# Kernel tuning notes

Hardware: AMD Instinct MI355X
Metric: run time of the kernel (lower is better)

Reference implementation:

```python
import jax, jax.numpy as jnp
import numpy as np

TEMPERATURE = 8.0  # sqrt(head_dim=64)
NEG_FILL = -1000000000.0

def setup_inputs() -> dict:
    key = jax.random.key(0)
    k1, k2, k3, k4, k5 = jax.random.split(key, 5)
    B, H, S, D = 4, 16, 1024, 64
    q = jax.random.normal(k1, (B, H, S, D), dtype=jnp.float32)
    k = jax.random.normal(k2, (B, H, S, D), dtype=jnp.float32)
    v = jax.random.normal(k3, (B, H, S, D), dtype=jnp.float32)
    similarity = jax.random.normal(k4, (B, H, S, S), dtype=jnp.float32)
    mask = jax.random.randint(k5, (B, 1, S, S), 0, 2).astype(bool)
    return {"q": q, "k": k, "v": v, "similarity": similarity, "mask": mask}

def reference(q, k, v, similarity, mask):
    # scores: [B,H,S,S] = (q/temp) @ k^T
    attn = jnp.einsum('bhqd,bhkd->bhqk', q / TEMPERATURE, k)
    attn = jnp.where(mask, NEG_FILL, attn)          # masked_fill (mask broadcasts over heads)
    attn = jax.nn.softmax(attn + similarity, axis=-1)  # dropout p=0 (eval): identity
    output = jnp.einsum('bhqk,bhkd->bhqd', attn, v)
    return (output, attn)
```

## Files before the change

### kernel.cpp

```cpp
#include <hip/hip_runtime.h>
#include <stdint.h>


#define S_LEN 1024
#define D_DIM 64
#define QT 16
#define SSTR 1032
#define NEG_FILL (-1000000000.0f)
#define LOG2E 1.44269504088896340736f

typedef __bf16 bf16x8 __attribute__((ext_vector_type(8)));
typedef float f32x4 __attribute__((ext_vector_type(4)));
typedef unsigned short u16x4 __attribute__((ext_vector_type(4)));
typedef unsigned short u16x8 __attribute__((ext_vector_type(8)));

__device__ __forceinline__ unsigned short f2bf(float x) {
    unsigned u = __builtin_bit_cast(unsigned, x);
    u += 0x7fffu + ((u >> 16) & 1u);
    return (unsigned short)(u >> 16);
}
__device__ __forceinline__ float bf2f(unsigned short b) {
    return __builtin_bit_cast(float, (unsigned)b << 16);
}

__global__ void prep_qkm(const float* __restrict__ q, const float* __restrict__ k,
                         const void* __restrict__ mraw,
                         unsigned short* __restrict__ Qb, unsigned short* __restrict__ Kb,
                         unsigned char* __restrict__ Mb)
{
    const int t = threadIdx.x;
    const int i = blockIdx.x * 256 + t;
    f32x4 q4 = ((const f32x4*)q)[i];
    f32x4 k4 = ((const f32x4*)k)[i];
    u16x4 qo, ko;
#pragma unroll
    for (int j = 0; j < 4; ++j) {
        qo[j] = f2bf(q4[j] * 0.125f);
        ko[j] = f2bf(k4[j]);
    }
    ((u16x4*)Qb)[i] = qo;
    ((u16x4*)Kb)[i] = ko;

    __shared__ int s_not_int, s_not_f32;
    if (t == 0) { s_not_int = 0; s_not_f32 = 0; }
    __syncthreads();
    const unsigned* wdd = (const unsigned*)mraw;
    int ni = 0, nf = 0;
    for (int j = t; j < 1024; j += 256) {
        unsigned x = wdd[j];
        if (x > 1u) ni = 1;
        if (x != 0u && x != 0x3f800000u) nf = 1;
    }
    if (ni) s_not_int = 1;
    if (nf) s_not_f32 = 1;
    __syncthreads();
    const int fmt = (s_not_int == 0) ? 0 : ((s_not_f32 == 0) ? 1 : 2);
    uchar4 o;
    if (fmt == 0) {
        int4 x = ((const int4*)mraw)[i];
        o.x = x.x ? 1 : 0; o.y = x.y ? 1 : 0; o.z = x.z ? 1 : 0; o.w = x.w ? 1 : 0;
    } else if (fmt == 1) {
        float4 x = ((const float4*)mraw)[i];
        o.x = (x.x != 0.f) ? 1 : 0; o.y = (x.y != 0.f) ? 1 : 0;
        o.z = (x.z != 0.f) ? 1 : 0; o.w = (x.w != 0.f) ? 1 : 0;
    } else {
        uchar4 x = ((const uchar4*)mraw)[i];
        o.x = x.x ? 1 : 0; o.y = x.y ? 1 : 0; o.z = x.z ? 1 : 0; o.w = x.w ? 1 : 0;
    }
    ((uchar4*)Mb)[i] = o;
}

__global__ void prep_vt(const float* __restrict__ v, unsigned short* __restrict__ Vt)
{
    __shared__ unsigned short sT[64 * 72];
    const int bh = blockIdx.x >> 4;
    const int st = blockIdx.x & 15;
    const int t = threadIdx.x;
    const float* vb = v + (size_t)(bh * S_LEN + st * 64) * D_DIM;
#pragma unroll
    for (int p = 0; p < 4; ++p) {
        int lin = p * 256 + t;
        int r = lin >> 4;
        int c = lin & 15;
        f32x4 x = ((const f32x4*)(vb + r * D_DIM))[c];
        unsigned short* dst = &sT[r * 72 + c * 4];
#pragma unroll
        for (int j = 0; j < 4; ++j) dst[j] = f2bf(x[j]);
    }
    __syncthreads();
    unsigned short* ob = Vt + (size_t)bh * D_DIM * S_LEN + st * 64;
#pragma unroll
    for (int p = 0; p < 4; ++p) {
        int lin = p * 256 + t;
        int d = lin >> 4;
        int s4 = (lin & 15) * 4;
        u16x4 o;
#pragma unroll
        for (int j = 0; j < 4; ++j) o[j] = sT[(s4 + j) * 72 + d];
        *(u16x4*)&ob[d * S_LEN + s4] = o;
    }
}

__global__ __launch_bounds__(256, 4)
void attn_main(const float* __restrict__ simg_, const unsigned short* __restrict__ Qb,
               const unsigned short* __restrict__ Kb, const unsigned short* __restrict__ Vtb,
               const unsigned char* __restrict__ Mb, float* __restrict__ out,
               float* __restrict__ attn)
{
    __shared__ __align__(16) unsigned short sS[QT * SSTR];

    const int blk = blockIdx.x;
    const int bh = blk >> 6;
    const int qt = blk & 63;
    const int b = bh >> 4;
    const int t = threadIdx.x;
    const int w = t >> 6;
    const int lane = t & 63;
    const int quad = lane >> 4;
    const int l15 = lane & 15;

    const unsigned short* Qg = Qb + (size_t)(bh * S_LEN + qt * QT) * D_DIM;
    const unsigned short* Kg = Kb + (size_t)bh * S_LEN * D_DIM;
    const unsigned short* Vg = Vtb + (size_t)bh * D_DIM * S_LEN;
    const float* simg = simg_ + ((size_t)(bh * S_LEN + qt * QT)) * S_LEN;
    const unsigned char* mg = Mb + ((size_t)(b * S_LEN + qt * QT)) * S_LEN;
    float* attng = attn + ((size_t)(bh * S_LEN + qt * QT)) * S_LEN;

    const int n0 = w * 16;
    const bf16x8 av0 = *(const bf16x8*)&Qg[l15 * D_DIM + quad * 8];
    const bf16x8 av1 = *(const bf16x8*)&Qg[l15 * D_DIM + 32 + quad * 8];
#pragma unroll 4
    for (int kt = 0; kt < 16; ++kt) {
        const unsigned short* kp = &Kg[(size_t)(kt * 64 + n0 + l15) * D_DIM + quad * 8];
        bf16x8 bv0 = *(const bf16x8*)kp;
        bf16x8 bv1 = *(const bf16x8*)(kp + 32);
        f32x4 acc = {0.f, 0.f, 0.f, 0.f};
        acc = __builtin_amdgcn_mfma_f32_16x16x32_bf16(av0, bv0, acc, 0, 0, 0);
        acc = __builtin_amdgcn_mfma_f32_16x16x32_bf16(av1, bv1, acc, 0, 0, 0);
        const int colg = kt * 64 + n0 + l15;
#pragma unroll
        for (int r = 0; r < 4; ++r)
            sS[(quad * 4 + r) * SSTR + colg] = f2bf(acc[r]);
    }
    __syncthreads();

#pragma unroll 1
    for (int rr = 0; rr < 4; ++rr) {
        const int row = w * 4 + rr;
        const float* sp = simg + (size_t)row * S_LEN;
        const unsigned char* mp = mg + (size_t)row * S_LEN;
        float vals[16];
        float mx = -3.0e38f;
#pragma unroll
        for (int j = 0; j < 4; ++j) {
            int col = j * 256 + lane * 4;
            u16x4 x = *(const u16x4*)&sS[row * SSTR + col];
            f32x4 sv = *(const f32x4*)&sp[col];
            uchar4 mk = *(const uchar4*)&mp[col];
            float f0 = mk.x ? NEG_FILL : (bf2f(x[0]) + sv[0]);
            float f1 = mk.y ? NEG_FILL : (bf2f(x[1]) + sv[1]);
            float f2 = mk.z ? NEG_FILL : (bf2f(x[2]) + sv[2]);
            float f3 = mk.w ? NEG_FILL : (bf2f(x[3]) + sv[3]);
            vals[j * 4 + 0] = f0; vals[j * 4 + 1] = f1;
            vals[j * 4 + 2] = f2; vals[j * 4 + 3] = f3;
            mx = fmaxf(mx, fmaxf(fmaxf(f0, f1), fmaxf(f2, f3)));
        }
#pragma unroll
        for (int off = 32; off > 0; off >>= 1)
            mx = fmaxf(mx, __shfl_xor(mx, off, 64));
        float sum = 0.f;
#pragma unroll
        for (int i = 0; i < 16; ++i) {
            float e = exp2f((vals[i] - mx) * LOG2E);
            vals[i] = e;
            sum += e;
        }
#pragma unroll
        for (int off = 32; off > 0; off >>= 1)
            sum += __shfl_xor(sum, off, 64);
        const float rinv = 1.0f / sum;
#pragma unroll
        for (int j = 0; j < 4; ++j) {
            int col = j * 256 + lane * 4;
            f32x4 p;
            u16x4 pb;
#pragma unroll
            for (int i = 0; i < 4; ++i) {
                float pi = vals[j * 4 + i] * rinv;
                p[i] = pi;
                pb[i] = f2bf(pi);
            }
            *(f32x4*)&attng[(size_t)row * S_LEN + col] = p;
            *(u16x4*)&sS[row * SSTR + col] = pb;
        }
    }
    __syncthreads();

    f32x4 oacc = {0.f, 0.f, 0.f, 0.f};
    const int d0 = w * 16;
#pragma unroll 4
    for (int kt = 0; kt < 16; ++kt) {
        const unsigned short* vp = &Vg[(size_t)(d0 + l15) * S_LEN + kt * 64 + quad * 8];
        bf16x8 bv0 = *(const bf16x8*)vp;
        bf16x8 bv1 = *(const bf16x8*)(vp + 32);
        bf16x8 pa0 = *(const bf16x8*)&sS[l15 * SSTR + kt * 64 + quad * 8];
        bf16x8 pa1 = *(const bf16x8*)&sS[l15 * SSTR + kt * 64 + 32 + quad * 8];
        oacc = __builtin_amdgcn_mfma_f32_16x16x32_bf16(pa0, bv0, oacc, 0, 0, 0);
        oacc = __builtin_amdgcn_mfma_f32_16x16x32_bf16(pa1, bv1, oacc, 0, 0, 0);
    }
    float* og = out + ((size_t)(bh * S_LEN + qt * QT)) * D_DIM;
#pragma unroll
    for (int r = 0; r < 4; ++r) {
        int row = quad * 4 + r;
        og[row * D_DIM + d0 + l15] = oacc[r];
    }
}

extern "C" void kernel_launch(void* const* d_in, const int* in_sizes, int n_in,
                              void* d_out, int out_size, void* d_ws, size_t ws_size,
                              hipStream_t stream)
{
    const float* q = (const float*)d_in[0];
    const float* k = (const float*)d_in[1];
    const float* v = (const float*)d_in[2];
    const float* sim = (const float*)d_in[3];
    const void* mask = d_in[4];
    float* out = (float*)d_out;
    float* attn = out + (size_t)4 * 16 * 1024 * 64;

    char* ws = (char*)d_ws;
    unsigned short* Qb = (unsigned short*)(ws + (size_t)0);
    unsigned short* Kb = (unsigned short*)(ws + ((size_t)8 << 20));
    unsigned short* Vt = (unsigned short*)(ws + ((size_t)16 << 20));
    unsigned char*  Mb = (unsigned char*)(ws + ((size_t)24 << 20));

    prep_qkm<<<4096, 256, 0, stream>>>(q, k, mask, Qb, Kb, Mb);
    prep_vt<<<1024, 256, 0, stream>>>(v, Vt);
    attn_main<<<4096, 256, 0, stream>>>(sim, Qb, Kb, Vt, Mb, out, attn);
}
```

Baseline: 574.3 us.

## Keep scores in registers, DMA similarity into LDS, swizzle P tile

Score tiles from QK^T now stay in registers, so the bf16 round trip through shared memory before softmax is gone and scores keep fp32 precision. Row max and sum are combined across waves with small LDS reductions. The similarity rows are prefetched with global_load_lds DMA that overlaps the QK MFMAs. The P tile goes into an XOR-swizzled LDS layout, the PV loop uses two accumulators, outputs are written with nontemporal stores, and block indices are remapped. Holding 64 accumulator values per thread raises register pressure, so launch bounds drop to 2 blocks per SM, and the attn writes become strided 4-byte scattered stores instead of 16-byte vector stores.

```diff
diff --git a/kernel.cpp b/kernel.cpp
--- a/kernel.cpp
+++ b/kernel.cpp
@@ -5,14 +5,13 @@
 #define S_LEN 1024
 #define D_DIM 64
 #define QT 16
-#define SSTR 1032
 #define NEG_FILL (-1000000000.0f)
 #define LOG2E 1.44269504088896340736f
+#define SIMSTR 4160
 
 typedef __bf16 bf16x8 __attribute__((ext_vector_type(8)));
 typedef float f32x4 __attribute__((ext_vector_type(4)));
 typedef unsigned short u16x4 __attribute__((ext_vector_type(4)));
-typedef unsigned short u16x8 __attribute__((ext_vector_type(8)));
 
 __device__ __forceinline__ unsigned short f2bf(float x) {
     unsigned u = __builtin_bit_cast(unsigned, x);
@@ -21,6 +20,16 @@
 }
 __device__ __forceinline__ float bf2f(unsigned short b) {
     return __builtin_bit_cast(float, (unsigned)b << 16);
+}
+
+__device__ __forceinline__ void dma16(const void* g, void* l) {
+    __builtin_amdgcn_global_load_lds(
+        (const __attribute__((address_space(1))) unsigned int*)g,
+        (__attribute__((address_space(3))) unsigned int*)l, 16, 0, 0);
+}
+
+__device__ __forceinline__ unsigned short* sptr(unsigned short* s, int row, int col) {
+    return (unsigned short*)((char*)s + row * 2048 + ((col * 2) ^ ((row & 7) << 4)));
 }
 
 __global__ void prep_qkm(const float* __restrict__ q, const float* __restrict__ k,
@@ -101,15 +110,15 @@
     }
 }
 
-__global__ __launch_bounds__(256, 4)
+__global__ __launch_bounds__(256, 2)
 void attn_main(const float* __restrict__ simg_, const unsigned short* __restrict__ Qb,
                const unsigned short* __restrict__ Kb, const unsigned short* __restrict__ Vtb,
                const unsigned char* __restrict__ Mb, float* __restrict__ out,
                float* __restrict__ attn)
 {
-    __shared__ __align__(16) unsigned short sS[QT * SSTR];
-
-    const int blk = blockIdx.x;
+    __shared__ __align__(16) unsigned char smem[16 * SIMSTR + 512];
+
+    const int blk = ((blockIdx.x & 7) << 9) | (blockIdx.x >> 3);
     const int bh = blk >> 6;
     const int qt = blk & 63;
     const int b = bh >> 4;
@@ -118,6 +127,7 @@
     const int lane = t & 63;
     const int quad = lane >> 4;
     const int l15 = lane & 15;
+    const int n0 = w * 16;
 
     const unsigned short* Qg = Qb + (size_t)(bh * S_LEN + qt * QT) * D_DIM;
     const unsigned short* Kg = Kb + (size_t)bh * S_LEN * D_DIM;
@@ -126,94 +136,142 @@
     const unsigned char* mg = Mb + ((size_t)(b * S_LEN + qt * QT)) * S_LEN;
     float* attng = attn + ((size_t)(bh * S_LEN + qt * QT)) * S_LEN;
 
-    const int n0 = w * 16;
+#pragma unroll
+    for (int rr = 0; rr < 4; ++rr) {
+        const float* gr = simg + (size_t)(w * 4 + rr) * S_LEN + lane * 4;
+        unsigned char* lr = smem + (w * 4 + rr) * SIMSTR;
+#pragma unroll
+        for (int c = 0; c < 4; ++c)
+            dma16(gr + c * 256, lr + c * 1024);
+    }
+
     const bf16x8 av0 = *(const bf16x8*)&Qg[l15 * D_DIM + quad * 8];
     const bf16x8 av1 = *(const bf16x8*)&Qg[l15 * D_DIM + 32 + quad * 8];
-#pragma unroll 4
+    f32x4 acc[16];
+#pragma unroll
     for (int kt = 0; kt < 16; ++kt) {
         const unsigned short* kp = &Kg[(size_t)(kt * 64 + n0 + l15) * D_DIM + quad * 8];
-        bf16x8 bv0 = *(const bf16x8*)kp;
-        bf16x8 bv1 = *(const bf16x8*)(kp + 32);
-        f32x4 acc = {0.f, 0.f, 0.f, 0.f};
-        acc = __builtin_amdgcn_mfma_f32_16x16x32_bf16(av0, bv0, acc, 0, 0, 0);
-        acc = __builtin_amdgcn_mfma_f32_16x16x32_bf16(av1, bv1, acc, 0, 0, 0);
-        const int colg = kt * 64 + n0 + l15;
+        bf16x8 kv0 = *(const bf16x8*)kp;
+        bf16x8 kv1 = *(const bf16x8*)(kp + 32);
+        f32x4 a = {0.f, 0.f, 0.f, 0.f};
+        a = __builtin_amdgcn_mfma_f32_16x16x32_bf16(av0, kv0, a, 0, 0, 0);
+        a = __builtin_amdgcn_mfma_f32_16x16x32_bf16(av1, kv1, a, 0, 0, 0);
+        acc[kt] = a;
+    }
+
+    unsigned char mk[16][4];
+#pragma unroll
+    for (int kt = 0; kt < 16; ++kt)
 #pragma unroll
         for (int r = 0; r < 4; ++r)
-            sS[(quad * 4 + r) * SSTR + colg] = f2bf(acc[r]);
-    }
-    __syncthreads();
-
-#pragma unroll 1
-    for (int rr = 0; rr < 4; ++rr) {
-        const int row = w * 4 + rr;
-        const float* sp = simg + (size_t)row * S_LEN;
-        const unsigned char* mp = mg + (size_t)row * S_LEN;
-        float vals[16];
-        float mx = -3.0e38f;
-#pragma unroll
-        for (int j = 0; j < 4; ++j) {
-            int col = j * 256 + lane * 4;
-            u16x4 x = *(const u16x4*)&sS[row * SSTR + col];
-            f32x4 sv = *(const f32x4*)&sp[col];
-            uchar4 mk = *(const uchar4*)&mp[col];
-            float f0 = mk.x ? NEG_FILL : (bf2f(x[0]) + sv[0]);
-            float f1 = mk.y ? NEG_FILL : (bf2f(x[1]) + sv[1]);
-            float f2 = mk.z ? NEG_FILL : (bf2f(x[2]) + sv[2]);
-            float f3 = mk.w ? NEG_FILL : (bf2f(x[3]) + sv[3]);
-            vals[j * 4 + 0] = f0; vals[j * 4 + 1] = f1;
-            vals[j * 4 + 2] = f2; vals[j * 4 + 3] = f3;
-            mx = fmaxf(mx, fmaxf(fmaxf(f0, f1), fmaxf(f2, f3)));
+            mk[kt][r] = mg[(size_t)(quad * 4 + r) * S_LEN + kt * 64 + n0 + l15];
+
+    __syncthreads();
+
+#pragma unroll
+    for (int kt = 0; kt < 16; ++kt)
+#pragma unroll
+        for (int r = 0; r < 4; ++r) {
+            float sv = *(const float*)(smem + (quad * 4 + r) * SIMSTR
+                                       + (size_t)(kt * 64 + n0 + l15) * 4);
+            acc[kt][r] = mk[kt][r] ? NEG_FILL : (acc[kt][r] + sv);
         }
-#pragma unroll
-        for (int off = 32; off > 0; off >>= 1)
-            mx = fmaxf(mx, __shfl_xor(mx, off, 64));
-        float sum = 0.f;
-#pragma unroll
-        for (int i = 0; i < 16; ++i) {
-            float e = exp2f((vals[i] - mx) * LOG2E);
-            vals[i] = e;
-            sum += e;
+
+    float* cmbMax = (float*)(smem + 16 * SIMSTR);
+    float* cmbSum = (float*)(smem + 16 * SIMSTR + 256);
+    float pm[4];
+#pragma unroll
+    for (int r = 0; r < 4; ++r) {
+        float m = acc[0][r];
+#pragma unroll
+        for (int kt = 1; kt < 16; ++kt) m = fmaxf(m, acc[kt][r]);
+#pragma unroll
+        for (int off = 1; off <= 8; off <<= 1)
+            m = fmaxf(m, __shfl_xor(m, off, 64));
+        pm[r] = m;
+    }
+    if (l15 == 0) {
+        f32x4 v = {pm[0], pm[1], pm[2], pm[3]};
+        *(f32x4*)&cmbMax[w * 16 + quad * 4] = v;
+    }
+    __syncthreads();
+    float rM[4];
+#pragma unroll
+    for (int r = 0; r < 4; ++r) {
+        const int row = quad * 4 + r;
+        rM[r] = fmaxf(fmaxf(cmbMax[row], cmbMax[16 + row]),
+                      fmaxf(cmbMax[32 + row], cmbMax[48 + row]));
+    }
+
+    float ps[4] = {0.f, 0.f, 0.f, 0.f};
+#pragma unroll
+    for (int kt = 0; kt < 16; ++kt)
+#pragma unroll
+        for (int r = 0; r < 4; ++r) {
+            float e = __builtin_amdgcn_exp2f((acc[kt][r] - rM[r]) * LOG2E);
+            acc[kt][r] = e;
+            ps[r] += e;
         }
 #pragma unroll
-        for (int off = 32; off > 0; off >>= 1)
-            sum += __shfl_xor(sum, off, 64);
-        const float rinv = 1.0f / sum;
-#pragma unroll
-        for (int j = 0; j < 4; ++j) {
-            int col = j * 256 + lane * 4;
-            f32x4 p;
-            u16x4 pb;
-#pragma unroll
-            for (int i = 0; i < 4; ++i) {
-                float pi = vals[j * 4 + i] * rinv;
-                p[i] = pi;
-                pb[i] = f2bf(pi);
-            }
-            *(f32x4*)&attng[(size_t)row * S_LEN + col] = p;
-            *(u16x4*)&sS[row * SSTR + col] = pb;
+    for (int r = 0; r < 4; ++r)
+#pragma unroll
+        for (int off = 1; off <= 8; off <<= 1)
+            ps[r] += __shfl_xor(ps[r], off, 64);
+    if (l15 == 0) {
+        f32x4 v = {ps[0], ps[1], ps[2], ps[3]};
+        *(f32x4*)&cmbSum[w * 16 + quad * 4] = v;
+    }
+    __syncthreads();
+    float rinv[4];
+#pragma unroll
+    for (int r = 0; r < 4; ++r) {
+        const int row = quad * 4 + r;
+        rinv[r] = 1.0f / ((cmbSum[row] + cmbSum[16 + row]) +
+                          (cmbSum[32 + row] + cmbSum[48 + row]));
+    }
+
+    unsigned short* pL = (unsigned short*)smem;
+#pragma unroll
+    for (int kt = 0; kt < 16; ++kt)
+#pragma unroll
+        for (int r = 0; r < 4; ++r) {
+            float p = acc[kt][r] * rinv[r];
+            acc[kt][r] = p;
+            *sptr(pL, quad * 4 + r, kt * 64 + n0 + l15) = f2bf(p);
         }
-    }
-    __syncthreads();
-
-    f32x4 oacc = {0.f, 0.f, 0.f, 0.f};
+    __syncthreads();
+
     const int d0 = w * 16;
-#pragma unroll 4
-    for (int kt = 0; kt < 16; ++kt) {
-        const unsigned short* vp = &Vg[(size_t)(d0 + l15) * S_LEN + kt * 64 + quad * 8];
-        bf16x8 bv0 = *(const bf16x8*)vp;
-        bf16x8 bv1 = *(const bf16x8*)(vp + 32);
-        bf16x8 pa0 = *(const bf16x8*)&sS[l15 * SSTR + kt * 64 + quad * 8];
-        bf16x8 pa1 = *(const bf16x8*)&sS[l15 * SSTR + kt * 64 + 32 + quad * 8];
-        oacc = __builtin_amdgcn_mfma_f32_16x16x32_bf16(pa0, bv0, oacc, 0, 0, 0);
-        oacc = __builtin_amdgcn_mfma_f32_16x16x32_bf16(pa1, bv1, oacc, 0, 0, 0);
-    }
+    f32x4 oa0 = {0.f, 0.f, 0.f, 0.f}, oa1 = {0.f, 0.f, 0.f, 0.f};
+#pragma unroll
+    for (int kt = 0; kt < 16; kt += 2) {
+        const unsigned short* vp0 = &Vg[(size_t)(d0 + l15) * S_LEN + kt * 64 + quad * 8];
+        bf16x8 x0 = *(const bf16x8*)vp0;
+        bf16x8 x1 = *(const bf16x8*)(vp0 + 32);
+        bf16x8 y0 = *(const bf16x8*)(vp0 + 64);
+        bf16x8 y1 = *(const bf16x8*)(vp0 + 96);
+        bf16x8 pa0 = *(const bf16x8*)sptr(pL, l15, kt * 64 + quad * 8);
+        bf16x8 pa1 = *(const bf16x8*)sptr(pL, l15, kt * 64 + 32 + quad * 8);
+        bf16x8 pb0 = *(const bf16x8*)sptr(pL, l15, kt * 64 + 64 + quad * 8);
+        bf16x8 pb1 = *(const bf16x8*)sptr(pL, l15, kt * 64 + 96 + quad * 8);
+        oa0 = __builtin_amdgcn_mfma_f32_16x16x32_bf16(pa0, x0, oa0, 0, 0, 0);
+        oa0 = __builtin_amdgcn_mfma_f32_16x16x32_bf16(pa1, x1, oa0, 0, 0, 0);
+        oa1 = __builtin_amdgcn_mfma_f32_16x16x32_bf16(pb0, y0, oa1, 0, 0, 0);
+        oa1 = __builtin_amdgcn_mfma_f32_16x16x32_bf16(pb1, y1, oa1, 0, 0, 0);
+    }
+    f32x4 oacc = oa0 + oa1;
+
     float* og = out + ((size_t)(bh * S_LEN + qt * QT)) * D_DIM;
 #pragma unroll
-    for (int r = 0; r < 4; ++r) {
-        int row = quad * 4 + r;
-        og[row * D_DIM + d0 + l15] = oacc[r];
-    }
+    for (int r = 0; r < 4; ++r)
+        __builtin_nontemporal_store(oacc[r], &og[(quad * 4 + r) * D_DIM + d0 + l15]);
+
+#pragma unroll
+    for (int kt = 0; kt < 16; ++kt)
+#pragma unroll
+        for (int r = 0; r < 4; ++r)
+            __builtin_nontemporal_store(acc[kt][r],
+                &attng[(size_t)(quad * 4 + r) * S_LEN + kt * 64 + n0 + l15]);
 }
 
 extern "C" void kernel_launch(void* const* d_in, const int* in_sizes, int n_in,
```

After: 620.5 us. 8.0% more time.
